# Kernel optimization log

Measured on AMD Instinct MI355X. Metric: run time of the kernel, lower is better.

Reference implementation:

```python
import jax, jax.numpy as jnp
import numpy as np

B, S, H = 1, 2048, 2048
NH, NKV, HD = 16, 4, 128          # heads, kv heads, head_dim
RHD = 64                          # rope head dim
QC, KVC = 1536, 512               # q / kv latent dims
EPS = 1e-6
SCALE = (HD + RHD) ** -0.5


def rms_norm(x, w):
    var = jnp.mean(x.astype(jnp.float32) ** 2, axis=-1, keepdims=True)
    return (x * jax.lax.rsqrt(var + EPS) * w).astype(x.dtype)


def rotate_half(x):
    x1, x2 = x[..., : x.shape[-1] // 2], x[..., x.shape[-1] // 2:]
    return jnp.concatenate([-x2, x1], axis=-1)


def apply_rope(q, k, cos, sin):
    cos = cos[:, None, :, :]  # [B,1,S,RHD]
    sin = sin[:, None, :, :]
    return q * cos + rotate_half(q) * sin, k * cos + rotate_half(k) * sin


def setup_inputs() -> dict:
    key = jax.random.key(0)
    ks = jax.random.split(key, 12)
    X = jax.random.normal(ks[0], (B, S, H), jnp.float32)
    # rotary tables
    inv_freq = 1.0 / (10000.0 ** (np.arange(0, RHD, 2, dtype=np.float32) / RHD))
    t = np.arange(S, dtype=np.float32)
    freqs = np.outer(t, inv_freq)               # [S, RHD/2]
    emb = np.concatenate([freqs, freqs], -1)    # [S, RHD]
    cos = jnp.asarray(np.cos(emb))[None].repeat(B, 0)
    sin = jnp.asarray(np.sin(emb))[None].repeat(B, 0)
    mask = jnp.tril(jnp.ones((S, S), jnp.int32))[None].repeat(B, 0)  # causal
    sc = lambda fan_in: 1.0 / np.sqrt(fan_in)
    return dict(
        X=X, cos=cos, sin=sin, mask=mask,
        w_down_q=jax.random.normal(ks[1], (H, QC), jnp.float32) * sc(H),
        w_up_q=jax.random.normal(ks[2], (QC, H), jnp.float32) * sc(QC),
        w_qr=jax.random.normal(ks[3], (QC, NH * RHD), jnp.float32) * sc(QC),
        w_down_kv=jax.random.normal(ks[4], (H, KVC), jnp.float32) * sc(H),
        w_up_k=jax.random.normal(ks[5], (KVC, NKV * HD), jnp.float32) * sc(KVC),
        w_up_v=jax.random.normal(ks[6], (KVC, NKV * HD), jnp.float32) * sc(KVC),
        w_kr=jax.random.normal(ks[7], (H, RHD), jnp.float32) * sc(H),
        w_o=jax.random.normal(ks[8], (H, H), jnp.float32) * sc(H),
        q_norm_w=jnp.ones((QC,), jnp.float32),
        k_norm_w=jnp.ones((KVC,), jnp.float32),
    )


def reference(X, cos, sin, mask, w_down_q, w_up_q, w_qr, w_down_kv,
              w_up_k, w_up_v, w_kr, w_o, q_norm_w, k_norm_w):
    bsz, q_len, _ = X.shape
    n_rep = NH // NKV
    # --- Q path: down-project, RMSNorm, up-project + rope branch ---
    cq = rms_norm(X @ w_down_q, q_norm_w)                    # [B,S,QC]
    qc = (cq @ w_up_q).reshape(bsz, q_len, NH, HD).transpose(0, 2, 1, 3)
    qr = (cq @ w_qr).reshape(bsz, q_len, NH, RHD).transpose(0, 2, 1, 3)
    # --- KV path ---
    ckv = rms_norm(X @ w_down_kv, k_norm_w)                  # [B,S,KVC]
    kc = (ckv @ w_up_k).reshape(bsz, q_len, NKV, HD).transpose(0, 2, 1, 3)
    kr = (X @ w_kr).reshape(bsz, q_len, 1, RHD).transpose(0, 2, 1, 3)
    kc = jnp.repeat(kc, n_rep, axis=1)                       # [B,NH,S,HD]
    kr = jnp.broadcast_to(kr, (bsz, NH, q_len, RHD))         # repeat_kv(kr, NH)
    qr, kr = apply_rope(qr, kr, cos, sin)
    query = jnp.concatenate([qc, qr], axis=-1)               # [B,NH,S,HD+RHD]
    key = jnp.concatenate([kc, kr], axis=-1)
    value = (ckv @ w_up_v).reshape(bsz, q_len, NKV, HD).transpose(0, 2, 1, 3)
    value = jnp.repeat(value, n_rep, axis=1)                 # [B,NH,S,HD]
    # --- attention ---
    scores = jnp.einsum('bhqd,bhkd->bhqk', query, key) * SCALE
    scores = jnp.where(mask[:, None] == 0, -1e9, scores)
    attn = jax.nn.softmax(scores, axis=-1)                   # dropout p=0
    ctx = jnp.einsum('bhqk,bhkd->bhqd', attn, value)
    ctx = ctx.transpose(0, 2, 1, 3).reshape(bsz, q_len, NH * HD)
    return ctx @ w_o, attn
```

## Files before the change

kernel.cpp:

```cpp
#include <hip/hip_runtime.h>
#include <stdint.h>

typedef __bf16 bf16;
typedef __bf16 bf16x8 __attribute__((ext_vector_type(8)));
typedef __bf16 bf16x4 __attribute__((ext_vector_type(4)));
typedef float f32x4 __attribute__((ext_vector_type(4)));

#define DEVFN static __device__ __forceinline__

constexpr int S = 2048, Hdim = 2048, NH = 16, NKV = 4, HD = 128, RHD = 64, QC = 1536, KVC = 512;
constexpr int QKD = HD + RHD;
constexpr int DN = 2112;
constexpr float RMS_EPS = 1e-6f;
constexpr float ATT_SCALE = 0.07216878364870323f;

DEVFN float wave_sum(float v) {
#pragma unroll
  for (int o = 32; o > 0; o >>= 1) v += __shfl_xor(v, o, 64);
  return v;
}
DEVFN float block_sum(float v) {
  __shared__ float red_s[4];
  v = wave_sum(v);
  int lane = threadIdx.x & 63, wid = threadIdx.x >> 6;
  if (lane == 0) red_s[wid] = v;
  __syncthreads();
  v = red_s[0] + red_s[1] + red_s[2] + red_s[3];
  __syncthreads();
  return v;
}

DEVFN void lgkm_barrier() {
  asm volatile("s_waitcnt lgkmcnt(0)" ::: "memory");
  __builtin_amdgcn_s_barrier();
}

DEVFN void gload16(const bf16* g, bf16* l) {
  __builtin_amdgcn_global_load_lds(
      (const __attribute__((address_space(1))) uint32_t*)g,
      (__attribute__((address_space(3))) uint32_t*)l, 16, 0, 0);
}

template <typename OT>
DEVFN void gemm_core_async(const bf16* __restrict__ A, const bf16* __restrict__ Bt,
                           OT* __restrict__ C, int N, int lda, int ldb, int ldc,
                           int m0, int n0, float scale, int kend) {
  __shared__ alignas(16) bf16 As[128 * 32];
  __shared__ alignas(16) bf16 Bs[128 * 32];
  const int t = threadIdx.x;
  const int lane = t & 63;
  const int wm = ((t >> 7) & 1) * 64;
  const int wn = ((t >> 6) & 1) * 64;
  const int lr = lane & 15;
  const int lk = (lane >> 4) * 8;
  const int srow = t >> 2;
  const int scol = (t & 3) * 8;
  const bf16* Ab = A + (size_t)(m0 + srow) * lda + scol;
  const bf16* Bb = Bt + (size_t)(n0 + srow) * ldb + scol;
  bf16* Al = As + t * 8;
  bf16* Bl = Bs + t * 8;

  f32x4 acc[4][4];
#pragma unroll
  for (int i = 0; i < 4; i++)
#pragma unroll
    for (int j = 0; j < 4; j++) { f32x4 z = {0.f, 0.f, 0.f, 0.f}; acc[i][j] = z; }

  for (int kk = 0; kk < kend; kk += 32) {
    gload16(Ab + kk, Al);
    gload16(Ab + (size_t)64 * lda + kk, Al + 2048);
    gload16(Bb + kk, Bl);
    gload16(Bb + (size_t)64 * ldb + kk, Bl + 2048);
    __syncthreads();
    bf16x8 a[4], b[4];
#pragma unroll
    for (int i = 0; i < 4; i++)
      a[i] = *reinterpret_cast<const bf16x8*>(&As[(wm + i * 16 + lr) * 32 + lk]);
#pragma unroll
    for (int i = 0; i < 4; i++)
      b[i] = *reinterpret_cast<const bf16x8*>(&Bs[(wn + i * 16 + lr) * 32 + lk]);
#pragma unroll
    for (int i = 0; i < 4; i++)
#pragma unroll
      for (int j = 0; j < 4; j++)
        acc[i][j] = __builtin_amdgcn_mfma_f32_16x16x32_bf16(a[i], b[j], acc[i][j], 0, 0, 0);
    __syncthreads();
  }
  const int orow = (lane >> 4) * 4;
#pragma unroll
  for (int i = 0; i < 4; i++) {
#pragma unroll
    for (int j = 0; j < 4; j++) {
      int col = n0 + wn + j * 16 + lr;
      if (col < N) {
#pragma unroll
        for (int q = 0; q < 4; q++) {
          int row = m0 + wm + i * 16 + orow + q;
          C[(size_t)row * ldc + col] = (OT)(acc[i][j][q] * scale);
        }
      }
    }
  }
}

template <typename OT>
__global__ __launch_bounds__(256) void gemm_nt(const bf16* __restrict__ A, const bf16* __restrict__ Bt,
                                               OT* __restrict__ C, int N, int K, int lda,
                                               int ldb, int ldc, float scale) {
  gemm_core_async<OT>(A, Bt, C, N, lda, ldb, ldc, blockIdx.y * 128, blockIdx.x * 128, scale, K);
}

__global__ __launch_bounds__(256) void gemm_up_both(const bf16* __restrict__ cqb,
                                                    const bf16* __restrict__ ckvb,
                                                    const bf16* __restrict__ wt_up1,
                                                    const bf16* __restrict__ wt_up2,
                                                    bf16* __restrict__ up1,
                                                    bf16* __restrict__ up2) {
  int id = blockIdx.x;
  if (id < 384) {
    gemm_core_async<bf16>(cqb, wt_up1, up1, 3072, QC, QC, 3072, (id / 24) * 128, (id % 24) * 128, 1.f, QC);
  } else {
    id -= 384;
    gemm_core_async<bf16>(ckvb, wt_up2, up2, 1024, KVC, KVC, 1024, (id / 8) * 128, (id % 8) * 128, 1.f, KVC);
  }
}

__global__ __launch_bounds__(512) void fa_fused(const bf16* __restrict__ qpack,
                                                const bf16* __restrict__ kpack,
                                                const bf16* __restrict__ vt,
                                                float* __restrict__ attn,
                                                bf16* __restrict__ ctxb) {
  const int h = blockIdx.y;
  const int g = h >> 2;
  __shared__ alignas(16) bf16 Ks[2][64 * 200];
  __shared__ alignas(16) bf16 Vs[3][128 * 72];
  __shared__ alignas(16) bf16 Ps[3][64 * 72];
  float2* sb = reinterpret_cast<float2*>(&Vs[0][0]);
  float2* statf = sb + 128;

  const int t = threadIdx.x;
  const int lane = t & 63;
  const int w = t >> 6;
  const int wm = (w & 3) * 16;
  const int kh = w >> 2;
  const int lr = lane & 15;
  const int hi = lane >> 4;
  const int lk = hi * 8;
  const int kr0 = t / 24, kc0 = (t % 24) * 8;
  const int kr1 = (t + 512) / 24, kc1 = ((t + 512) % 24) * 8;
  const int kr2 = (t + 1024) / 24, kc2 = ((t + 1024) % 24) * 8;
  const int vr0 = t >> 3, vc0 = (t & 7) * 8;
  const int vr1 = (t + 512) >> 3, vc1 = ((t + 512) & 7) * 8;

  const bf16* Qg = qpack + (size_t)h * S * QKD;
  const bf16* Kg = kpack + (size_t)g * S * QKD;
  const bf16* Vg = vt + (size_t)g * HD * S;
  float* Ah = attn + (size_t)h * S * S;
  bf16* C = ctxb + h * HD;

  for (int sub = 0; sub < 2; ++sub) {
    const int m0 = sub ? (1984 - 64 * blockIdx.x) : (64 * blockIdx.x);
    const int ntiles = sub ? (32 - blockIdx.x) : (blockIdx.x + 1);
    const int kend = m0 + 64;
    __syncthreads();

    bf16x8 qf[6];
#pragma unroll
    for (int ks = 0; ks < 6; ++ks)
      qf[ks] = *reinterpret_cast<const bf16x8*>(&Qg[(size_t)(m0 + wm + lr) * QKD + ks * 32 + lk]);

    float mreg[4] = {-1e30f, -1e30f, -1e30f, -1e30f};
    float lreg[4] = {0.f, 0.f, 0.f, 0.f};
    bf16x8 ck0 = *reinterpret_cast<const bf16x8*>(&Kg[(size_t)kr0 * QKD + kc0]);
    bf16x8 ck1 = *reinterpret_cast<const bf16x8*>(&Kg[(size_t)kr1 * QKD + kc1]);
    bf16x8 ck2 = *reinterpret_cast<const bf16x8*>(&Kg[(size_t)kr2 * QKD + kc2]);
    int cur = 0;
    for (int ti = 0; ti < ntiles; ++ti) {
      const int kt = ti * 64;
      bf16x8 nk0, nk1, nk2;
      if (ti + 1 < ntiles) {
        nk0 = *reinterpret_cast<const bf16x8*>(&Kg[(size_t)(kt + 64 + kr0) * QKD + kc0]);
        nk1 = *reinterpret_cast<const bf16x8*>(&Kg[(size_t)(kt + 64 + kr1) * QKD + kc1]);
        nk2 = *reinterpret_cast<const bf16x8*>(&Kg[(size_t)(kt + 64 + kr2) * QKD + kc2]);
      }
      *reinterpret_cast<bf16x8*>(&Ks[cur][kr0 * 200 + kc0]) = ck0;
      *reinterpret_cast<bf16x8*>(&Ks[cur][kr1 * 200 + kc1]) = ck1;
      *reinterpret_cast<bf16x8*>(&Ks[cur][kr2 * 200 + kc2]) = ck2;
      lgkm_barrier();
      f32x4 acc[2];
#pragma unroll
      for (int kb = 0; kb < 2; kb++) { f32x4 z = {0.f, 0.f, 0.f, 0.f}; acc[kb] = z; }
#pragma unroll
      for (int ks = 0; ks < 6; ++ks) {
#pragma unroll
        for (int kb = 0; kb < 2; ++kb) {
          bf16x8 b = *reinterpret_cast<const bf16x8*>(&Ks[cur][(kh * 32 + kb * 16 + lr) * 200 + ks * 32 + lk]);
          acc[kb] = __builtin_amdgcn_mfma_f32_16x16x32_bf16(qf[ks], b, acc[kb], 0, 0, 0);
        }
      }
      const int colb = kt + kh * 32 + lr;
#pragma unroll
      for (int q = 0; q < 4; ++q) {
        const int rowg = m0 + wm + hi * 4 + q;
        bool u0 = (colb <= rowg), u1 = (colb + 16 <= rowg);
        float s0 = u0 ? acc[0][q] * ATT_SCALE : -1e30f;
        float s1 = u1 ? acc[1][q] * ATT_SCALE : -1e30f;
        float nm = fmaxf(mreg[q], fmaxf(s0, s1));
        float e0 = u0 ? __expf(s0 - nm) : 0.f;
        float e1 = u1 ? __expf(s1 - nm) : 0.f;
        lreg[q] = lreg[q] * __expf(mreg[q] - nm) + e0 + e1;
        mreg[q] = nm;
      }
      ck0 = nk0; ck1 = nk1; ck2 = nk2;
      cur ^= 1;
    }
#pragma unroll
    for (int q = 0; q < 4; ++q) {
      float m = mreg[q], l = lreg[q];
#pragma unroll
      for (int o = 1; o < 16; o <<= 1) {
        float mo = __shfl_xor(m, o, 64);
        float lo = __shfl_xor(l, o, 64);
        float M = fmaxf(m, mo);
        l = l * __expf(m - M) + lo * __expf(mo - M);
        m = M;
      }
      mreg[q] = m; lreg[q] = l;
    }
    __syncthreads();
    if (lr == 0) {
#pragma unroll
      for (int q = 0; q < 4; ++q)
        sb[kh * 64 + wm + hi * 4 + q] = make_float2(mreg[q], lreg[q]);
    }
    __syncthreads();
    if (w < 4 && lr == 0) {
#pragma unroll
      for (int q = 0; q < 4; ++q) {
        int r = wm + hi * 4 + q;
        float2 a = sb[r], b = sb[64 + r];
        float M = fmaxf(a.x, b.x);
        float L = a.y * __expf(a.x - M) + b.y * __expf(b.x - M);
        statf[r] = make_float2(M, 1.0f / L);
      }
    }
    __syncthreads();
    float mr[4], invl[4];
#pragma unroll
    for (int q = 0; q < 4; ++q) {
      float2 sv = statf[wm + hi * 4 + q];
      mr[q] = sv.x; invl[q] = sv.y;
    }
    __syncthreads();

    f32x4 accp[4];
#pragma unroll
    for (int j = 0; j < 4; j++) { f32x4 z = {0.f, 0.f, 0.f, 0.f}; accp[j] = z; }
    ck0 = *reinterpret_cast<const bf16x8*>(&Kg[(size_t)kr0 * QKD + kc0]);
    ck1 = *reinterpret_cast<const bf16x8*>(&Kg[(size_t)kr1 * QKD + kc1]);
    ck2 = *reinterpret_cast<const bf16x8*>(&Kg[(size_t)kr2 * QKD + kc2]);
    bf16x8 cv0 = *reinterpret_cast<const bf16x8*>(&Vg[(size_t)vr0 * S + vc0]);
    bf16x8 cv1 = *reinterpret_cast<const bf16x8*>(&Vg[(size_t)vr1 * S + vc1]);
    cur = 0;
    int pb = 0;
    for (int ti = 0; ti < ntiles; ++ti) {
      const int kt = ti * 64;
      bf16x8 nk0, nk1, nk2, nv0, nv1;
      if (ti + 1 < ntiles) {
        nk0 = *reinterpret_cast<const bf16x8*>(&Kg[(size_t)(kt + 64 + kr0) * QKD + kc0]);
        nk1 = *reinterpret_cast<const bf16x8*>(&Kg[(size_t)(kt + 64 + kr1) * QKD + kc1]);
        nk2 = *reinterpret_cast<const bf16x8*>(&Kg[(size_t)(kt + 64 + kr2) * QKD + kc2]);
        nv0 = *reinterpret_cast<const bf16x8*>(&Vg[(size_t)vr0 * S + kt + 64 + vc0]);
        nv1 = *reinterpret_cast<const bf16x8*>(&Vg[(size_t)vr1 * S + kt + 64 + vc1]);
      }
      *reinterpret_cast<bf16x8*>(&Ks[cur][kr0 * 200 + kc0]) = ck0;
      *reinterpret_cast<bf16x8*>(&Ks[cur][kr1 * 200 + kc1]) = ck1;
      *reinterpret_cast<bf16x8*>(&Ks[cur][kr2 * 200 + kc2]) = ck2;
      *reinterpret_cast<bf16x8*>(&Vs[pb][vr0 * 72 + vc0]) = cv0;
      *reinterpret_cast<bf16x8*>(&Vs[pb][vr1 * 72 + vc1]) = cv1;
      lgkm_barrier();
      f32x4 acc[2];
#pragma unroll
      for (int kb = 0; kb < 2; kb++) { f32x4 z = {0.f, 0.f, 0.f, 0.f}; acc[kb] = z; }
#pragma unroll
      for (int ks = 0; ks < 6; ++ks) {
#pragma unroll
        for (int kb = 0; kb < 2; ++kb) {
          bf16x8 b = *reinterpret_cast<const bf16x8*>(&Ks[cur][(kh * 32 + kb * 16 + lr) * 200 + ks * 32 + lk]);
          acc[kb] = __builtin_amdgcn_mfma_f32_16x16x32_bf16(qf[ks], b, acc[kb], 0, 0, 0);
        }
      }
      const int colb = kt + kh * 32 + lr;
#pragma unroll
      for (int kb = 0; kb < 2; ++kb) {
#pragma unroll
        for (int q = 0; q < 4; ++q) {
          const int rloc = wm + hi * 4 + q;
          const int rowg = m0 + rloc;
          const int col = colb + kb * 16;
          float s = acc[kb][q] * ATT_SCALE;
          float p = (col <= rowg) ? __expf(s - mr[q]) * invl[q] : 0.f;
          Ah[(size_t)rowg * S + col] = p;
          Ps[pb][rloc * 72 + kh * 32 + kb * 16 + lr] = (bf16)p;
        }
      }
      if (ti > 0) {
        const int pp = (pb == 0) ? 2 : pb - 1;
#pragma unroll
        for (int ks = 0; ks < 2; ++ks) {
          bf16x8 a = *reinterpret_cast<const bf16x8*>(&Ps[pp][(wm + lr) * 72 + ks * 32 + lk]);
#pragma unroll
          for (int j = 0; j < 4; ++j) {
            bf16x8 b = *reinterpret_cast<const bf16x8*>(&Vs[pp][(kh * 64 + j * 16 + lr) * 72 + ks * 32 + lk]);
            accp[j] = __builtin_amdgcn_mfma_f32_16x16x32_bf16(a, b, accp[j], 0, 0, 0);
          }
        }
      }
      ck0 = nk0; ck1 = nk1; ck2 = nk2; cv0 = nv0; cv1 = nv1;
      cur ^= 1;
      pb = (pb == 2) ? 0 : pb + 1;
    }
    lgkm_barrier();
    {
      const int pp = (pb == 0) ? 2 : pb - 1;
#pragma unroll
      for (int ks = 0; ks < 2; ++ks) {
        bf16x8 a = *reinterpret_cast<const bf16x8*>(&Ps[pp][(wm + lr) * 72 + ks * 32 + lk]);
#pragma unroll
        for (int j = 0; j < 4; ++j) {
          bf16x8 b = *reinterpret_cast<const bf16x8*>(&Vs[pp][(kh * 64 + j * 16 + lr) * 72 + ks * 32 + lk]);
          accp[j] = __builtin_amdgcn_mfma_f32_16x16x32_bf16(a, b, accp[j], 0, 0, 0);
        }
      }
    }

    const float4 zz = make_float4(0.f, 0.f, 0.f, 0.f);
    {
      const int zr = t >> 3, zc0 = (t & 7) * 4;
      float* zrow = Ah + (size_t)(m0 + zr) * S;
      for (int k = kend + zc0; k < S; k += 32) *reinterpret_cast<float4*>(zrow + k) = zz;
    }

#pragma unroll
    for (int j = 0; j < 4; ++j) {
      const int d = kh * 64 + j * 16 + lr;
#pragma unroll
      for (int q = 0; q < 4; ++q) {
        const int rowg = m0 + wm + hi * 4 + q;
        C[(size_t)rowg * Hdim + d] = (bf16)accp[j][q];
      }
    }
  }
}

struct TJobs {
  const float* src[8];
  bf16* dst[8];
  int R[8], C[8], tiles[8];
};

__global__ __launch_bounds__(256) void prep(const float* __restrict__ Xf,
                                            bf16* __restrict__ Xb, TJobs J) {
  const int t = threadIdx.x;
  int id = blockIdx.x;
  if (id < 2048) {
    size_t i = (size_t)id * 256 + t;
    float4 f0 = *reinterpret_cast<const float4*>(Xf + i * 8);
    float4 f1 = *reinterpret_cast<const float4*>(Xf + i * 8 + 4);
    bf16x8 v;
    v[0] = (bf16)f0.x; v[1] = (bf16)f0.y; v[2] = (bf16)f0.z; v[3] = (bf16)f0.w;
    v[4] = (bf16)f1.x; v[5] = (bf16)f1.y; v[6] = (bf16)f1.z; v[7] = (bf16)f1.w;
    *reinterpret_cast<bf16x8*>(Xb + i * 8) = v;
    return;
  }
  int tile = id - 2048;
  int j = 0;
  while (tile >= J.tiles[j]) { tile -= J.tiles[j]; ++j; }
  const int C = J.C[j], R = J.R[j];
  int tcn = C >> 5;
  int rb = (tile / tcn) * 32, cb = (tile % tcn) * 32;
  const float* in = J.src[j];
  bf16* out = J.dst[j];
  __shared__ float tl[32][33];
  int tx = t & 31, ty = t >> 5;
#pragma unroll
  for (int q = 0; q < 32; q += 8)
    tl[ty + q][tx] = in[(size_t)(rb + ty + q) * C + cb + tx];
  __syncthreads();
#pragma unroll
  for (int q = 0; q < 32; q += 8)
    out[(size_t)(cb + ty + q) * R + rb + tx] = (bf16)tl[tx][ty + q];
}

__global__ __launch_bounds__(256) void rmsnorm_fused(const float* __restrict__ dproj,
                                                     const float* __restrict__ qw,
                                                     const float* __restrict__ kw,
                                                     bf16* __restrict__ cqb,
                                                     bf16* __restrict__ ckvb) {
  int row = blockIdx.x;
  bool isq = (blockIdx.y == 0);
  int C = isq ? QC : KVC;
  const float* p = dproj + (size_t)row * DN + (isq ? 0 : QC);
  const float* w = isq ? qw : kw;
  bf16* out = (isq ? cqb : ckvb) + (size_t)row * C;
  float ss = 0.f;
  for (int i = threadIdx.x * 4; i < C; i += 1024) {
    float4 v = *reinterpret_cast<const float4*>(p + i);
    ss += v.x * v.x + v.y * v.y + v.z * v.z + v.w * v.w;
  }
  ss = block_sum(ss);
  float r = rsqrtf(ss / (float)C + RMS_EPS);
  for (int i = threadIdx.x * 4; i < C; i += 1024) {
    float4 v = *reinterpret_cast<const float4*>(p + i);
    float4 g = *reinterpret_cast<const float4*>(w + i);
    bf16x4 o;
    o[0] = (bf16)(v.x * r * g.x); o[1] = (bf16)(v.y * r * g.y);
    o[2] = (bf16)(v.z * r * g.z); o[3] = (bf16)(v.w * r * g.w);
    *reinterpret_cast<bf16x4*>(out + i) = o;
  }
}

__global__ __launch_bounds__(256) void pack_all(const bf16* __restrict__ up1,
                                                const bf16* __restrict__ up2,
                                                const float* __restrict__ dproj,
                                                const float* __restrict__ cosp,
                                                const float* __restrict__ sinp,
                                                bf16* __restrict__ qpack,
                                                bf16* __restrict__ kpack,
                                                bf16* __restrict__ vt) {
  const int t = threadIdx.x;
  int id = blockIdx.x;
  if (id < 3072) {
    int idx = id * 256 + t;
    const int P = NH * S * 16;
    if (idx < P) {
      int d8 = idx & 15, s = (idx >> 4) & (S - 1), h = idx >> 15;
      int4 v = *reinterpret_cast<const int4*>(up1 + (size_t)s * 3072 + h * HD + d8 * 8);
      *reinterpret_cast<int4*>(qpack + ((size_t)h * S + s) * QKD + d8 * 8) = v;
    } else {
      int j = idx - P;
      int d0 = (j & 7) * 8, s = (j >> 3) & (S - 1), h = j >> 14;
      const bf16* xr = up1 + (size_t)s * 3072 + 2048 + h * RHD;
      bf16x8 xa = *reinterpret_cast<const bf16x8*>(xr + d0);
      bf16x8 xb = *reinterpret_cast<const bf16x8*>(xr + (d0 ^ 32));
      float sign = (d0 < 32) ? -1.f : 1.f;
      const float* cr = cosp + s * RHD + d0;
      const float* sr = sinp + s * RHD + d0;
      bf16x8 o;
#pragma unroll
      for (int i = 0; i < 8; i++)
        o[i] = (bf16)((float)xa[i] * cr[i] + sign * (float)xb[i] * sr[i]);
      *reinterpret_cast<bf16x8*>(qpack + ((size_t)h * S + s) * QKD + HD + d0) = o;
    }
    return;
  }
  if (id < 3648) {
    int idx = (id - 3072) * 256 + t;
    const int P = NKV * S * 16;
    if (idx < P) {
      int d8 = idx & 15, s = (idx >> 4) & (S - 1), g = idx >> 15;
      int4 v = *reinterpret_cast<const int4*>(up2 + (size_t)s * 1024 + g * HD + d8 * 8);
      *reinterpret_cast<int4*>(kpack + ((size_t)g * S + s) * QKD + d8 * 8) = v;
    } else {
      int j = idx - P;
      int d0 = (j & 7) * 8, s = j >> 3;
      const float* xr = dproj + (size_t)s * DN + 2048;
      float4 a0 = *reinterpret_cast<const float4*>(xr + d0);
      float4 a1 = *reinterpret_cast<const float4*>(xr + d0 + 4);
      float4 b0 = *reinterpret_cast<const float4*>(xr + (d0 ^ 32));
      float4 b1 = *reinterpret_cast<const float4*>(xr + (d0 ^ 32) + 4);
      float sign = (d0 < 32) ? -1.f : 1.f;
      const float* cr = cosp + s * RHD + d0;
      const float* sr = sinp + s * RHD + d0;
      float xa[8] = {a0.x, a0.y, a0.z, a0.w, a1.x, a1.y, a1.z, a1.w};
      float xb[8] = {b0.x, b0.y, b0.z, b0.w, b1.x, b1.y, b1.z, b1.w};
      bf16x8 o;
#pragma unroll
      for (int i = 0; i < 8; i++)
        o[i] = (bf16)(xa[i] * cr[i] + sign * xb[i] * sr[i]);
#pragma unroll
      for (int g = 0; g < NKV; g++)
        *reinterpret_cast<bf16x8*>(kpack + ((size_t)g * S + s) * QKD + HD + d0) = o;
    }
    return;
  }
  int tile = id - 3648;
  int cb = (tile & 15) * 32;
  int rb = (tile >> 4) * 32;
  __shared__ float tl[32][33];
  int tx = t & 31, ty = t >> 5;
  const bf16* in = up2 + 512;
#pragma unroll
  for (int q = 0; q < 32; q += 8)
    tl[ty + q][tx] = (float)in[(size_t)(rb + ty + q) * 1024 + cb + tx];
  __syncthreads();
#pragma unroll
  for (int q = 0; q < 32; q += 8)
    vt[(size_t)(cb + ty + q) * S + rb + tx] = (bf16)tl[tx][ty + q];
}

extern "C" void kernel_launch(void* const* d_in, const int* in_sizes, int n_in, void* d_out,
                              int out_size, void* d_ws, size_t ws_size, hipStream_t stream) {
  const float* Xf = (const float*)d_in[0];
  const float* cosp = (const float*)d_in[1];
  const float* sinp = (const float*)d_in[2];
  const float* w_down_q = (const float*)d_in[4];
  const float* w_up_q = (const float*)d_in[5];
  const float* w_qr = (const float*)d_in[6];
  const float* w_down_kv = (const float*)d_in[7];
  const float* w_up_k = (const float*)d_in[8];
  const float* w_up_v = (const float*)d_in[9];
  const float* w_kr = (const float*)d_in[10];
  const float* w_o = (const float*)d_in[11];
  const float* q_norm_w = (const float*)d_in[12];
  const float* k_norm_w = (const float*)d_in[13];

  float* out0 = (float*)d_out;
  float* attn = out0 + (size_t)S * Hdim;

  char* base = (char*)d_ws;
  size_t off = 0;
  auto carve = [&](size_t bytes) -> void* {
    void* p = base + off;
    off += (bytes + 255) & ~(size_t)255;
    return p;
  };
  bf16* Xb      = (bf16*)carve((size_t)S * Hdim * 2);
  bf16* wt_down = (bf16*)carve((size_t)2176 * 2048 * 2);
  bf16* wt_up1  = (bf16*)carve((size_t)3072 * QC * 2);
  bf16* wt_up2  = (bf16*)carve((size_t)1024 * KVC * 2);
  bf16* wt_o    = (bf16*)carve((size_t)Hdim * Hdim * 2);
  float* dproj  = (float*)carve((size_t)S * DN * 4);
  bf16* cqb     = (bf16*)carve((size_t)S * QC * 2);
  bf16* ckvb    = (bf16*)carve((size_t)S * KVC * 2);
  bf16* up1     = (bf16*)carve((size_t)S * 3072 * 2);
  bf16* up2     = (bf16*)carve((size_t)S * 1024 * 2);
  bf16* qpack   = (bf16*)carve((size_t)NH * S * QKD * 2);
  bf16* kpack   = (bf16*)carve((size_t)NKV * S * QKD * 2);
  bf16* vt      = (bf16*)carve((size_t)NKV * HD * S * 2);
  bf16* ctxb    = (bf16*)carve((size_t)S * Hdim * 2);
  (void)in_sizes; (void)n_in; (void)out_size; (void)ws_size;

  TJobs J;
  const float* srcs[8] = {w_down_q, w_down_kv, w_kr, w_up_q, w_qr, w_up_k, w_up_v, w_o};
  bf16* dsts[8] = {wt_down, wt_down + (size_t)QC * 2048, wt_down + (size_t)2048 * 2048,
                   wt_up1, wt_up1 + (size_t)2048 * QC, wt_up2, wt_up2 + (size_t)512 * KVC, wt_o};
  int Rs[8] = {2048, 2048, 2048, 1536, 1536, 512, 512, 2048};
  int Cs[8] = {1536, 512, 64, 2048, 1024, 512, 512, 2048};
  int total_tiles = 0;
  for (int j = 0; j < 8; j++) {
    J.src[j] = srcs[j]; J.dst[j] = dsts[j]; J.R[j] = Rs[j]; J.C[j] = Cs[j];
    J.tiles[j] = (Rs[j] / 32) * (Cs[j] / 32);
    total_tiles += J.tiles[j];
  }

  prep<<<2048 + total_tiles, 256, 0, stream>>>(Xf, Xb, J);
  gemm_nt<float><<<dim3(17, 16), 256, 0, stream>>>(Xb, wt_down, dproj, DN, Hdim, Hdim, Hdim, DN, 1.f);
  rmsnorm_fused<<<dim3(S, 2), 256, 0, stream>>>(dproj, q_norm_w, k_norm_w, cqb, ckvb);
  gemm_up_both<<<512, 256, 0, stream>>>(cqb, ckvb, wt_up1, wt_up2, up1, up2);
  pack_all<<<4672, 256, 0, stream>>>(up1, up2, dproj, cosp, sinp, qpack, kpack, vt);
  fa_fused<<<dim3(16, NH), 512, 0, stream>>>(qpack, kpack, vt, attn, ctxb);
  gemm_nt<float><<<dim3(16, 16), 256, 0, stream>>>(ctxb, wt_o, out0, Hdim, Hdim, Hdim, Hdim, Hdim, 1.f);
}
```

Before: 310.0 us.

## Double-buffer GEMM tiles via register prefetch and raise priority around MFMA blocks

The GEMM core drops the direct global-to-LDS loads with two barriers per k-step. It now prefetches the next k-slice into registers while computing on a double-buffered LDS tile, so only one barrier is needed per step. s_setprio is also raised around the MFMA sections in both the GEMM and the attention kernels, to favour matrix issue across waves. This doubles GEMM LDS use, which may reduce occupancy, and adds VGPR pressure for the prefetch registers.

```diff
diff --git a/kernel.cpp b/kernel.cpp
--- a/kernel.cpp
+++ b/kernel.cpp
@@ -35,18 +35,12 @@
   __builtin_amdgcn_s_barrier();
 }
 
-DEVFN void gload16(const bf16* g, bf16* l) {
-  __builtin_amdgcn_global_load_lds(
-      (const __attribute__((address_space(1))) uint32_t*)g,
-      (__attribute__((address_space(3))) uint32_t*)l, 16, 0, 0);
-}
-
 template <typename OT>
-DEVFN void gemm_core_async(const bf16* __restrict__ A, const bf16* __restrict__ Bt,
-                           OT* __restrict__ C, int N, int lda, int ldb, int ldc,
-                           int m0, int n0, float scale, int kend) {
-  __shared__ alignas(16) bf16 As[128 * 32];
-  __shared__ alignas(16) bf16 Bs[128 * 32];
+DEVFN void gemm_core_pipe(const bf16* __restrict__ A, const bf16* __restrict__ Bt,
+                          OT* __restrict__ C, int N, int lda, int ldb, int ldc,
+                          int m0, int n0, float scale, int kend) {
+  __shared__ alignas(16) bf16 As[2][128 * 32];
+  __shared__ alignas(16) bf16 Bs[2][128 * 32];
   const int t = threadIdx.x;
   const int lane = t & 63;
   const int wm = ((t >> 7) & 1) * 64;
@@ -55,10 +49,10 @@
   const int lk = (lane >> 4) * 8;
   const int srow = t >> 2;
   const int scol = (t & 3) * 8;
-  const bf16* Ab = A + (size_t)(m0 + srow) * lda + scol;
-  const bf16* Bb = Bt + (size_t)(n0 + srow) * ldb + scol;
-  bf16* Al = As + t * 8;
-  bf16* Bl = Bs + t * 8;
+  const bf16* A0 = A + (size_t)(m0 + srow) * lda + scol;
+  const bf16* A1 = A + (size_t)(m0 + 64 + srow) * lda + scol;
+  const bf16* B0 = Bt + (size_t)(n0 + srow) * ldb + scol;
+  const bf16* B1 = Bt + (size_t)(n0 + 64 + srow) * ldb + scol;
 
   f32x4 acc[4][4];
 #pragma unroll
@@ -66,25 +60,40 @@
 #pragma unroll
     for (int j = 0; j < 4; j++) { f32x4 z = {0.f, 0.f, 0.f, 0.f}; acc[i][j] = z; }
 
+  bf16x8 ca0 = *reinterpret_cast<const bf16x8*>(A0);
+  bf16x8 ca1 = *reinterpret_cast<const bf16x8*>(A1);
+  bf16x8 cb0 = *reinterpret_cast<const bf16x8*>(B0);
+  bf16x8 cb1 = *reinterpret_cast<const bf16x8*>(B1);
+  int cur = 0;
   for (int kk = 0; kk < kend; kk += 32) {
-    gload16(Ab + kk, Al);
-    gload16(Ab + (size_t)64 * lda + kk, Al + 2048);
-    gload16(Bb + kk, Bl);
-    gload16(Bb + (size_t)64 * ldb + kk, Bl + 2048);
-    __syncthreads();
+    bf16x8 na0, na1, nb0, nb1;
+    if (kk + 32 < kend) {
+      na0 = *reinterpret_cast<const bf16x8*>(A0 + kk + 32);
+      na1 = *reinterpret_cast<const bf16x8*>(A1 + kk + 32);
+      nb0 = *reinterpret_cast<const bf16x8*>(B0 + kk + 32);
+      nb1 = *reinterpret_cast<const bf16x8*>(B1 + kk + 32);
+    }
+    *reinterpret_cast<bf16x8*>(&As[cur][t * 8]) = ca0;
+    *reinterpret_cast<bf16x8*>(&As[cur][t * 8 + 2048]) = ca1;
+    *reinterpret_cast<bf16x8*>(&Bs[cur][t * 8]) = cb0;
+    *reinterpret_cast<bf16x8*>(&Bs[cur][t * 8 + 2048]) = cb1;
+    lgkm_barrier();
     bf16x8 a[4], b[4];
 #pragma unroll
     for (int i = 0; i < 4; i++)
-      a[i] = *reinterpret_cast<const bf16x8*>(&As[(wm + i * 16 + lr) * 32 + lk]);
+      a[i] = *reinterpret_cast<const bf16x8*>(&As[cur][(wm + i * 16 + lr) * 32 + lk]);
 #pragma unroll
     for (int i = 0; i < 4; i++)
-      b[i] = *reinterpret_cast<const bf16x8*>(&Bs[(wn + i * 16 + lr) * 32 + lk]);
+      b[i] = *reinterpret_cast<const bf16x8*>(&Bs[cur][(wn + i * 16 + lr) * 32 + lk]);
+    __builtin_amdgcn_s_setprio(1);
 #pragma unroll
     for (int i = 0; i < 4; i++)
 #pragma unroll
       for (int j = 0; j < 4; j++)
         acc[i][j] = __builtin_amdgcn_mfma_f32_16x16x32_bf16(a[i], b[j], acc[i][j], 0, 0, 0);
-    __syncthreads();
+    __builtin_amdgcn_s_setprio(0);
+    ca0 = na0; ca1 = na1; cb0 = nb0; cb1 = nb1;
+    cur ^= 1;
   }
   const int orow = (lane >> 4) * 4;
 #pragma unroll
@@ -107,7 +116,7 @@
 __global__ __launch_bounds__(256) void gemm_nt(const bf16* __restrict__ A, const bf16* __restrict__ Bt,
                                                OT* __restrict__ C, int N, int K, int lda,
                                                int ldb, int ldc, float scale) {
-  gemm_core_async<OT>(A, Bt, C, N, lda, ldb, ldc, blockIdx.y * 128, blockIdx.x * 128, scale, K);
+  gemm_core_pipe<OT>(A, Bt, C, N, lda, ldb, ldc, blockIdx.y * 128, blockIdx.x * 128, scale, K);
 }
 
 __global__ __launch_bounds__(256) void gemm_up_both(const bf16* __restrict__ cqb,
@@ -118,10 +127,10 @@
                                                     bf16* __restrict__ up2) {
   int id = blockIdx.x;
   if (id < 384) {
-    gemm_core_async<bf16>(cqb, wt_up1, up1, 3072, QC, QC, 3072, (id / 24) * 128, (id % 24) * 128, 1.f, QC);
+    gemm_core_pipe<bf16>(cqb, wt_up1, up1, 3072, QC, QC, 3072, (id / 24) * 128, (id % 24) * 128, 1.f, QC);
   } else {
     id -= 384;
-    gemm_core_async<bf16>(ckvb, wt_up2, up2, 1024, KVC, KVC, 1024, (id / 8) * 128, (id % 8) * 128, 1.f, KVC);
+    gemm_core_pipe<bf16>(ckvb, wt_up2, up2, 1024, KVC, KVC, 1024, (id / 8) * 128, (id % 8) * 128, 1.f, KVC);
   }
 }
 
@@ -190,6 +199,7 @@
       f32x4 acc[2];
 #pragma unroll
       for (int kb = 0; kb < 2; kb++) { f32x4 z = {0.f, 0.f, 0.f, 0.f}; acc[kb] = z; }
+      __builtin_amdgcn_s_setprio(1);
 #pragma unroll
       for (int ks = 0; ks < 6; ++ks) {
 #pragma unroll
@@ -198,6 +208,7 @@
           acc[kb] = __builtin_amdgcn_mfma_f32_16x16x32_bf16(qf[ks], b, acc[kb], 0, 0, 0);
         }
       }
+      __builtin_amdgcn_s_setprio(0);
       const int colb = kt + kh * 32 + lr;
 #pragma unroll
       for (int q = 0; q < 4; ++q) {
@@ -282,6 +293,7 @@
       f32x4 acc[2];
 #pragma unroll
       for (int kb = 0; kb < 2; kb++) { f32x4 z = {0.f, 0.f, 0.f, 0.f}; acc[kb] = z; }
+      __builtin_amdgcn_s_setprio(1);
 #pragma unroll
       for (int ks = 0; ks < 6; ++ks) {
 #pragma unroll
@@ -290,6 +302,7 @@
           acc[kb] = __builtin_amdgcn_mfma_f32_16x16x32_bf16(qf[ks], b, acc[kb], 0, 0, 0);
         }
       }
+      __builtin_amdgcn_s_setprio(0);
       const int colb = kt + kh * 32 + lr;
 #pragma unroll
       for (int kb = 0; kb < 2; ++kb) {
@@ -306,6 +319,7 @@
       }
       if (ti > 0) {
         const int pp = (pb == 0) ? 2 : pb - 1;
+        __builtin_amdgcn_s_setprio(1);
 #pragma unroll
         for (int ks = 0; ks < 2; ++ks) {
           bf16x8 a = *reinterpret_cast<const bf16x8*>(&Ps[pp][(wm + lr) * 72 + ks * 32 + lk]);
@@ -315,6 +329,7 @@
             accp[j] = __builtin_amdgcn_mfma_f32_16x16x32_bf16(a, b, accp[j], 0, 0, 0);
           }
         }
+        __builtin_amdgcn_s_setprio(0);
       }
       ck0 = nk0; ck1 = nk1; ck2 = nk2; cv0 = nv0; cv1 = nv1;
       cur ^= 1;
```

After: 306.8 us (median of 2 runs). About the same (-1.1%).
